# Optimization experiments

Hardware: AMD Instinct MI355X
Metric: run time of the kernel (lower is better)

The kernel has to match this reference:

```python
import jax, jax.numpy as jnp
import numpy as np

# Dropout layers are treated as identity (eval mode); note the original Adaptive
# module references self.dropout without defining it, so train mode would error anyway.

def setup_inputs() -> dict:
    key = jax.random.key(0)
    ks = jax.random.split(key, 13)
    B, T, H, E2, VOC, K = 128, 64, 512, 1024, 10000, 49
    s = lambda *sh: 1.0 / np.sqrt(sh[-1])
    return {
        "x":       jax.random.normal(ks[0], (B, T, E2), jnp.float32),
        "hiddens": jax.random.normal(ks[1], (B, T, H), jnp.float32),
        "cells":   jax.random.normal(ks[2], (B, T, H), jnp.float32),
        "V":       jax.random.normal(ks[3], (B, K, H), jnp.float32),
        # attention params
        "Wv": jax.random.normal(ks[4], (K, H), jnp.float32) * s(K, H),
        "Wg": jax.random.normal(ks[5], (K, H), jnp.float32) * s(K, H),
        "Ws": jax.random.normal(ks[6], (K, H), jnp.float32) * s(K, H),
        "wh": jax.random.normal(ks[7], (K,), jnp.float32) * s(K,),
        # sentinel params
        "Wx":  jax.random.normal(ks[8], (H, E2), jnp.float32) * s(H, E2),
        "Wsh": jax.random.normal(ks[9], (H, H), jnp.float32) * s(H, H),
        # output mlp
        "Wm": jax.random.normal(ks[10], (VOC, H), jnp.float32) * s(VOC, H),
        "bm": jnp.zeros((VOC,), jnp.float32),
    }


def reference(x, hiddens, cells, V, Wv, Wg, Ws, wh, Wx, Wsh, Wm, bm):
    B, T, H = hiddens.shape
    # h_{t-1}: zero init state prepended, last hidden dropped
    h0 = jnp.zeros((B, 1, H), hiddens.dtype)
    hiddens_t_1 = jnp.concatenate([h0, hiddens[:, :-1, :]], axis=1) if T > 1 else h0

    # Sentinel gate: sent_t = sigmoid(x Wx^T + h_{t-1} Wh^T) * tanh(cells)
    gate = jnp.einsum('bte,he->bth', x, Wx) + jnp.einsum('btj,hj->bth', hiddens_t_1, Wsh)
    sent = jax.nn.sigmoid(gate) * jnp.tanh(cells)            # [B,T,H]

    # Additive attention over K=49 spatial features
    cv = jnp.einsum('bkh,nh->bkn', V, Wv)                    # [B,K,49]
    cg = jnp.einsum('bth,nh->btn', hiddens, Wg)              # [B,T,49]
    content = jnp.tanh(cv[:, None, :, :] + cg[:, :, None, :])  # [B,T,K,49]
    z = jnp.einsum('btkn,n->btk', content, wh)               # [B,T,K]
    alpha = jax.nn.softmax(z, axis=-1)                       # [B,T,K]
    c = jnp.einsum('btk,bkh->bth', alpha, V)                 # [B,T,H]

    # Sentinel-extended softmax -> beta
    cs = jnp.einsum('bth,nh->btn', sent, Ws) + cg            # [B,T,49]
    z_ext = jnp.einsum('btn,n->bt', jnp.tanh(cs), wh)[..., None]  # [B,T,1]
    extend = jnp.concatenate([z, z_ext], axis=-1)            # [B,T,K+1]
    alpha_hat = jax.nn.softmax(extend, axis=-1)
    beta = alpha_hat[:, :, -1:]                              # [B,T,1]

    c_hat = beta * sent + (1.0 - beta) * c                   # [B,T,H]
    output = jnp.einsum('bth,vh->btv', c_hat + hiddens, Wm) + bm  # [B,T,vocab]
    return output, alpha, beta
```

## Files before the change

### kernel.cpp

```cpp
#include <hip/hip_runtime.h>
#include <hip/hip_bf16.h>
#include <math.h>

typedef __bf16 bf16;
typedef __bf16 bf16x4 __attribute__((ext_vector_type(4)));
typedef __bf16 bf16x8 __attribute__((ext_vector_type(8)));
typedef float f32x4 __attribute__((ext_vector_type(4)));

#define BB  128
#define TT  64
#define BTT 8192
#define HH  512
#define EE  1024
#define KA  49
#define NV  10000

__device__ __forceinline__ float ftanh(float x) {
    float cx = fminf(fmaxf(x, -15.f), 15.f);
    float e = __expf(2.f * cx);
    return (e - 1.f) * __builtin_amdgcn_rcpf(e + 1.f);
}
__device__ __forceinline__ float fsigmoid(float x) {
    return __builtin_amdgcn_rcpf(1.f + __expf(-x));
}

__device__ __forceinline__ void cvt4(const float* __restrict__ s, bf16* __restrict__ d) {
    f32x4 v = *(const f32x4*)s;
    bf16x4 o = { (bf16)v[0], (bf16)v[1], (bf16)v[2], (bf16)v[3] };
    *(bf16x4*)d = o;
}
__device__ __forceinline__ void cvt4nt(const float* __restrict__ s, bf16* __restrict__ d) {
    f32x4 v = __builtin_nontemporal_load((const f32x4*)s);
    bf16x4 o = { (bf16)v[0], (bf16)v[1], (bf16)v[2], (bf16)v[3] };
    *(bf16x4*)d = o;
}

__global__ __launch_bounds__(256)
void prep_kernel(const float* __restrict__ hid,
                 const float* __restrict__ V, const float* __restrict__ Wv,
                 const float* __restrict__ Wg, const float* __restrict__ Ws,
                 const float* __restrict__ Wx, const float* __restrict__ Wsh,
                 bf16* __restrict__ hb,
                 bf16* __restrict__ Vb, bf16* __restrict__ Wvb, bf16* __restrict__ Wgb,
                 bf16* __restrict__ Wsb, bf16* __restrict__ Wxb, bf16* __restrict__ Wshb,
                 bf16* __restrict__ zbuf)
{
    if (blockIdx.x == 0 && threadIdx.x < 128) {
        bf16x8 z = {};
        *(bf16x8*)(zbuf + threadIdx.x * 8) = z;
    }

    const long NH = (long)BTT * HH;
    const long NVV = (long)BB * KA * HH;
    const long NWX = (long)HH * EE;
    const long NWSH = (long)HH * HH;
    const long NW = (long)KA * HH;
    const long total4 = (NH + NVV + NWX + NWSH + 3 * NW) >> 2;

    long t0 = (long)blockIdx.x * 256 + threadIdx.x;
    long st = (long)gridDim.x * 256;
    for (long i4 = t0; i4 < total4; i4 += st) {
        long i = i4 << 2;
        if (i < NH) { cvt4(hid + i, hb + i); continue; }
        i -= NH;
        if (i < NVV) { cvt4nt(V + i, Vb + i); continue; }
        i -= NVV;
        if (i < NWX) { cvt4nt(Wx + i, Wxb + i); continue; }
        i -= NWX;
        if (i < NWSH) { cvt4nt(Wsh + i, Wshb + i); continue; }
        i -= NWSH;
        if (i < NW) { cvt4nt(Wv + i, Wvb + i); continue; }
        i -= NW;
        if (i < NW) { cvt4nt(Wg + i, Wgb + i); continue; }
        i -= NW;
        cvt4nt(Ws + i, Wsb + i);
    }
}

template<int EPI, bool SHIFT>
__device__ __forceinline__ void gemm128_core(
    bf16* smem,
    const bf16* __restrict__ A1, const bf16* __restrict__ B1, int K1,
    const bf16* __restrict__ A2, const bf16* __restrict__ B2, int K2,
    int N, const float* __restrict__ eaux, void* __restrict__ outv, int ldo,
    int bm0, int bn0, const bf16* __restrict__ zbuf)
{
    const int tid = threadIdx.x;
    const int lane = tid & 63;
    const int wid = tid >> 6;
    const int wm = (wid >> 1) * 64;
    const int wn = (wid & 1) * 64;
    const int rA = lane & 15;
    const int ks = lane >> 4;
    const int swzB = (ks ^ ((rA >> 1) & 3)) * 16;

    const int c0 = tid, c1 = tid + 256;
    const int row0 = c0 >> 2, row1 = c1 >> 2;
    const int gc0 = ((c0 & 3) ^ ((row0 >> 1) & 3)) * 8;
    const int gc1 = ((c1 & 3) ^ ((row1 >> 1) & 3)) * 8;
    const int br0 = (bn0 + row0 < N) ? bn0 + row0 : N - 1;
    const int br1 = (bn0 + row1 < N) ? bn0 + row1 : N - 1;

    const int NT1 = K1 >> 5;
    const int NT2 = K2 >> 5;
    const int NT = NT1 + NT2;

    const bf16* A1r0 = A1 + (size_t)(bm0 + row0) * K1 + gc0;
    const bf16* A1r1 = A1 + (size_t)(bm0 + row1) * K1 + gc1;
    const bf16* B1r0 = B1 + (size_t)br0 * K1 + gc0;
    const bf16* B1r1 = B1 + (size_t)br1 * K1 + gc1;
    const bf16 *A2r0 = nullptr, *A2r1 = nullptr, *B2r0 = nullptr, *B2r1 = nullptr;
    if (K2 > 0) {
        if (SHIFT) {
            A2r0 = (((bm0 + row0) & 63) == 0) ? zbuf + gc0
                                              : A2 + (size_t)(bm0 + row0 - 1) * K2 + gc0;
            A2r1 = (((bm0 + row1) & 63) == 0) ? zbuf + gc1
                                              : A2 + (size_t)(bm0 + row1 - 1) * K2 + gc1;
        } else {
            A2r0 = A2 + (size_t)(bm0 + row0) * K2 + gc0;
            A2r1 = A2 + (size_t)(bm0 + row1) * K2 + gc1;
        }
        B2r0 = B2 + (size_t)br0 * K2 + gc0;
        B2r1 = B2 + (size_t)br1 * K2 + gc1;
    }

    auto stage = [&](int t) {
        const bf16 *a0, *a1, *b0, *b1; int k0;
        if (t < NT1) { k0 = t << 5;          a0 = A1r0; a1 = A1r1; b0 = B1r0; b1 = B1r1; }
        else         { k0 = (t - NT1) << 5;  a0 = A2r0; a1 = A2r1; b0 = B2r0; b1 = B2r1; }
        char* base = (char*)smem + (t & 3) * 16384;
        __builtin_amdgcn_global_load_lds(
            (const __attribute__((address_space(1))) unsigned int*)(a0 + k0),
            (__attribute__((address_space(3))) unsigned int*)(base + c0 * 16), 16, 0, 0);
        __builtin_amdgcn_global_load_lds(
            (const __attribute__((address_space(1))) unsigned int*)(a1 + k0),
            (__attribute__((address_space(3))) unsigned int*)(base + c1 * 16), 16, 0, 0);
        __builtin_amdgcn_global_load_lds(
            (const __attribute__((address_space(1))) unsigned int*)(b0 + k0),
            (__attribute__((address_space(3))) unsigned int*)(base + 8192 + c0 * 16), 16, 0, 0);
        __builtin_amdgcn_global_load_lds(
            (const __attribute__((address_space(1))) unsigned int*)(b1 + k0),
            (__attribute__((address_space(3))) unsigned int*)(base + 8192 + c1 * 16), 16, 0, 0);
    };

    f32x4 acc[4][4] = {};

    stage(0); stage(1); stage(2);
    asm volatile("s_waitcnt vmcnt(8)" ::: "memory");
    __builtin_amdgcn_s_barrier();

    for (int t = 0; t < NT; ++t) {
        const char* sA = (const char*)smem + (t & 3) * 16384;
        const char* sB = sA + 8192;

        bf16x8 af[4], bfr[4];
        #pragma unroll
        for (int mi = 0; mi < 4; ++mi)
            af[mi] = *(const bf16x8*)(sA + (wm + mi * 16 + rA) * 64 + swzB);
        #pragma unroll
        for (int ni = 0; ni < 4; ++ni)
            bfr[ni] = *(const bf16x8*)(sB + (wn + ni * 16 + rA) * 64 + swzB);

        if (t + 3 < NT) {
            stage(t + 3);
            asm volatile("s_waitcnt vmcnt(8)" ::: "memory");
        } else if (t + 2 < NT) {
            asm volatile("s_waitcnt vmcnt(4)" ::: "memory");
        } else {
            asm volatile("s_waitcnt vmcnt(0)" ::: "memory");
        }
        __builtin_amdgcn_s_barrier();

        __builtin_amdgcn_s_setprio(1);
        #pragma unroll
        for (int mi = 0; mi < 4; ++mi) {
            #pragma unroll
            for (int ni = 0; ni < 4; ++ni)
                acc[mi][ni] = __builtin_amdgcn_mfma_f32_16x16x32_bf16(af[mi], bfr[ni], acc[mi][ni], 0, 0, 0);
        }
        __builtin_amdgcn_s_setprio(0);
        __builtin_amdgcn_s_barrier();
    }

    #pragma unroll
    for (int mi = 0; mi < 4; ++mi) {
        #pragma unroll
        for (int ni = 0; ni < 4; ++ni) {
            const int col = bn0 + wn + ni * 16 + rA;
            if (col < N) {
                #pragma unroll
                for (int r = 0; r < 4; ++r) {
                    const int rowg = bm0 + wm + mi * 16 + ks * 4 + r;
                    float v = acc[mi][ni][r];
                    if (EPI == 0) {
                        ((bf16*)outv)[(size_t)rowg * ldo + col] =
                            (bf16)(fsigmoid(v) * ftanh(eaux[(size_t)rowg * ldo + col]));
                    } else {
                        ((float*)outv)[(size_t)rowg * ldo + col] = v;
                    }
                }
            }
        }
    }
}

__device__ __forceinline__ void gate128f(
    char* smem, const float* __restrict__ xf, const bf16* __restrict__ Wxb,
    const bf16* __restrict__ hb, const bf16* __restrict__ Wshb,
    const float* __restrict__ cel, bf16* __restrict__ sentb,
    int bm0, int bn0, const bf16* __restrict__ zbuf)
{
    const int NT1 = EE >> 5;
    const int NT = NT1 + (HH >> 5);

    const int tid = threadIdx.x;
    const int lane = tid & 63;
    const int wid = tid >> 6;
    const int wm = (wid >> 1) * 64;
    const int wn = (wid & 1) * 64;
    const int rA = lane & 15;
    const int ks = lane >> 4;
    const int swzB = (ks ^ ((rA >> 1) & 3)) * 16;

    const float* xsrc[4];
    #pragma unroll
    for (int j = 0; j < 4; ++j) {
        const int c = tid + 256 * j;
        const int row = c >> 3, slot = c & 7;
        xsrc[j] = xf + (size_t)(bm0 + row) * EE + ((slot ^ ((row >> 1) & 7)) << 2);
    }
    const int cb0 = tid, cb1 = tid + 256;
    const int brow0 = cb0 >> 2, brow1 = cb1 >> 2;
    const int gb0 = ((cb0 & 3) ^ ((brow0 >> 1) & 3)) * 8;
    const int gb1 = ((cb1 & 3) ^ ((brow1 >> 1) & 3)) * 8;

    const bf16* B1r0 = Wxb + (size_t)(bn0 + brow0) * EE + gb0;
    const bf16* B1r1 = Wxb + (size_t)(bn0 + brow1) * EE + gb1;
    const bf16* B2r0 = Wshb + (size_t)(bn0 + brow0) * HH + gb0;
    const bf16* B2r1 = Wshb + (size_t)(bn0 + brow1) * HH + gb1;
    const bf16* A2r0 = (((bm0 + brow0) & 63) == 0) ? zbuf + gb0
                                                   : hb + (size_t)(bm0 + brow0 - 1) * HH + gb0;
    const bf16* A2r1 = (((bm0 + brow1) & 63) == 0) ? zbuf + gb1
                                                   : hb + (size_t)(bm0 + brow1 - 1) * HH + gb1;

    auto stage = [&](int t, int slot) {
        char* base = smem + slot * 24576;
        if (t < NT1) {
            const int k0 = t << 5;
            #pragma unroll
            for (int j = 0; j < 4; ++j)
                __builtin_amdgcn_global_load_lds(
                    (const __attribute__((address_space(1))) unsigned int*)(xsrc[j] + k0),
                    (__attribute__((address_space(3))) unsigned int*)(base + (tid + 256 * j) * 16), 16, 0, 0);
            __builtin_amdgcn_global_load_lds(
                (const __attribute__((address_space(1))) unsigned int*)(B1r0 + k0),
                (__attribute__((address_space(3))) unsigned int*)(base + 16384 + cb0 * 16), 16, 0, 0);
            __builtin_amdgcn_global_load_lds(
                (const __attribute__((address_space(1))) unsigned int*)(B1r1 + k0),
                (__attribute__((address_space(3))) unsigned int*)(base + 16384 + cb1 * 16), 16, 0, 0);
        } else {
            const int k0 = (t - NT1) << 5;
            __builtin_amdgcn_global_load_lds(
                (const __attribute__((address_space(1))) unsigned int*)(A2r0 + k0),
                (__attribute__((address_space(3))) unsigned int*)(base + cb0 * 16), 16, 0, 0);
            __builtin_amdgcn_global_load_lds(
                (const __attribute__((address_space(1))) unsigned int*)(A2r1 + k0),
                (__attribute__((address_space(3))) unsigned int*)(base + cb1 * 16), 16, 0, 0);
            __builtin_amdgcn_global_load_lds(
                (const __attribute__((address_space(1))) unsigned int*)(B2r0 + k0),
                (__attribute__((address_space(3))) unsigned int*)(base + 16384 + cb0 * 16), 16, 0, 0);
            __builtin_amdgcn_global_load_lds(
                (const __attribute__((address_space(1))) unsigned int*)(B2r1 + k0),
                (__attribute__((address_space(3))) unsigned int*)(base + 16384 + cb1 * 16), 16, 0, 0);
        }
    };

    f32x4 acc[4][4] = {};

    stage(0, 0); stage(1, 1);
    asm volatile("s_waitcnt vmcnt(6)" ::: "memory");
    __builtin_amdgcn_s_barrier();

    int slR = 0, slS = 2;
    for (int t = 0; t < NT; ++t) {
        const char* base = smem + slR * 24576;
        const char* sB = base + 16384;

        bf16x8 af[4], bfr[4];
        if (t < NT1) {
            #pragma unroll
            for (int mi = 0; mi < 4; ++mi) {
                const int row = wm + mi * 16 + rA;
                const int m = (row >> 1) & 7;
                f32x4 lo = *(const f32x4*)(base + row * 128 + (((2 * ks) ^ m) << 4));
                f32x4 hi = *(const f32x4*)(base + row * 128 + (((2 * ks + 1) ^ m) << 4));
                bf16x8 v = { (bf16)lo[0], (bf16)lo[1], (bf16)lo[2], (bf16)lo[3],
                             (bf16)hi[0], (bf16)hi[1], (bf16)hi[2], (bf16)hi[3] };
                af[mi] = v;
            }
        } else {
            #pragma unroll
            for (int mi = 0; mi < 4; ++mi)
                af[mi] = *(const bf16x8*)(base + (wm + mi * 16 + rA) * 64 + swzB);
        }
        #pragma unroll
        for (int ni = 0; ni < 4; ++ni)
            bfr[ni] = *(const bf16x8*)(sB + (wn + ni * 16 + rA) * 64 + swzB);

        if (t + 2 < NT) {
            stage(t + 2, slS);
            if (t + 2 < NT1) asm volatile("s_waitcnt vmcnt(6)" ::: "memory");
            else             asm volatile("s_waitcnt vmcnt(4)" ::: "memory");
        } else {
            asm volatile("s_waitcnt vmcnt(0)" ::: "memory");
        }
        __builtin_amdgcn_s_barrier();

        __builtin_amdgcn_s_setprio(1);
        #pragma unroll
        for (int mi = 0; mi < 4; ++mi) {
            #pragma unroll
            for (int ni = 0; ni < 4; ++ni)
                acc[mi][ni] = __builtin_amdgcn_mfma_f32_16x16x32_bf16(af[mi], bfr[ni], acc[mi][ni], 0, 0, 0);
        }
        __builtin_amdgcn_s_setprio(0);
        __builtin_amdgcn_s_barrier();

        slR = (slR == 2) ? 0 : slR + 1;
        slS = (slS == 2) ? 0 : slS + 1;
    }

    #pragma unroll
    for (int mi = 0; mi < 4; ++mi) {
        #pragma unroll
        for (int ni = 0; ni < 4; ++ni) {
            const int col = bn0 + wn + ni * 16 + rA;
            #pragma unroll
            for (int r = 0; r < 4; ++r) {
                const int rowg = bm0 + wm + mi * 16 + ks * 4 + r;
                sentb[(size_t)rowg * HH + col] =
                    (bf16)(fsigmoid(acc[mi][ni][r]) * ftanh(cel[(size_t)rowg * HH + col]));
            }
        }
    }
}

__global__ __launch_bounds__(256, 2)
void gate_mid128(const float* __restrict__ xf, const bf16* __restrict__ Wxb,
                 const bf16* __restrict__ Wshb,
                 const float* __restrict__ cel, bf16* __restrict__ sentb,
                 const bf16* __restrict__ Vb, const bf16* __restrict__ Wvb,
                 const bf16* __restrict__ hb, const bf16* __restrict__ Wgb,
                 float* __restrict__ cv, float* __restrict__ cg,
                 const float* __restrict__ Wm, bf16* __restrict__ Wmb,
                 const bf16* __restrict__ zbuf)
{
    __shared__ char smem[73728];
    const int bid = blockIdx.x;
    if (bid >= 369) {
        const long n4 = ((long)NV * HH) >> 2;
        for (long i4 = (long)(bid - 369) * 256 + threadIdx.x; i4 < n4; i4 += 143L * 256)
            cvt4nt(Wm + (i4 << 2), Wmb + (i4 << 2));
        return;
    }
    if (bid < 256) {
        const int lin = (bid & 7) * 32 + (bid >> 3);
        gate128f(smem, xf, Wxb, hb, Wshb, cel, sentb,
                 (lin >> 2) * 128, (lin & 3) * 128, zbuf);
    } else if (bid < 305) {
        gemm128_core<2, false>((bf16*)smem, Vb, Wvb, HH, nullptr, nullptr, 0, KA, nullptr,
                               (void*)cv, KA, (bid - 256) * 128, 0, nullptr);
    } else {
        gemm128_core<2, false>((bf16*)smem, hb, Wgb, HH, nullptr, nullptr, 0, KA, nullptr,
                               (void*)cg, KA, (bid - 305) * 128, 0, nullptr);
    }
}

__global__ __launch_bounds__(256, 2)
void cs64(const bf16* __restrict__ sentb, const bf16* __restrict__ Wsb,
          float* __restrict__ cs)
{
    __shared__ bf16 smem[4 * 4096];
    const int bm0 = blockIdx.x * 64;
    const int tid = threadIdx.x;
    const int lane = tid & 63;
    const int w = tid >> 6;
    const int rA = lane & 15;
    const int ks = lane >> 4;
    const int swzB = (ks ^ ((rA >> 1) & 3)) * 16;

    const int row = tid >> 2;
    const int gc = ((tid & 3) ^ ((row >> 1) & 3)) * 8;
    const int browc = (row < KA) ? row : KA - 1;
    const bf16* Ar = sentb + (size_t)(bm0 + row) * HH + gc;
    const bf16* Br = Wsb + (size_t)browc * HH + gc;

    auto stage = [&](int t) {
        char* base = (char*)smem + (t & 3) * 8192;
        const int k0 = t << 5;
        __builtin_amdgcn_global_load_lds(
            (const __attribute__((address_space(1))) unsigned int*)(Ar + k0),
            (__attribute__((address_space(3))) unsigned int*)(base + tid * 16), 16, 0, 0);
        __builtin_amdgcn_global_load_lds(
            (const __attribute__((address_space(1))) unsigned int*)(Br + k0),
            (__attribute__((address_space(3))) unsigned int*)(base + 4096 + tid * 16), 16, 0, 0);
    };

    f32x4 acc[4] = {};
    const int NT = HH / 32;

    stage(0); stage(1); stage(2);
    asm volatile("s_waitcnt vmcnt(4)" ::: "memory");
    __builtin_amdgcn_s_barrier();

    for (int t = 0; t < NT; ++t) {
        const char* sA = (const char*)smem + (t & 3) * 8192;
        const char* sB = sA + 4096;

        bf16x8 af[4];
        #pragma unroll
        for (int mi = 0; mi < 4; ++mi)
            af[mi] = *(const bf16x8*)(sA + (mi * 16 + rA) * 64 + swzB);
        bf16x8 bfr = *(const bf16x8*)(sB + (w * 16 + rA) * 64 + swzB);

        if (t + 3 < NT) {
            stage(t + 3);
            asm volatile("s_waitcnt vmcnt(4)" ::: "memory");
        } else if (t + 2 < NT) {
            asm volatile("s_waitcnt vmcnt(2)" ::: "memory");
        } else {
            asm volatile("s_waitcnt vmcnt(0)" ::: "memory");
        }
        __builtin_amdgcn_s_barrier();

        __builtin_amdgcn_s_setprio(1);
        #pragma unroll
        for (int mi = 0; mi < 4; ++mi)
            acc[mi] = __builtin_amdgcn_mfma_f32_16x16x32_bf16(af[mi], bfr, acc[mi], 0, 0, 0);
        __builtin_amdgcn_s_setprio(0);
        __builtin_amdgcn_s_barrier();
    }

    const int col = w * 16 + rA;
    if (col < KA) {
        #pragma unroll
        for (int mi = 0; mi < 4; ++mi) {
            #pragma unroll
            for (int r = 0; r < 4; ++r) {
                const int rowg = bm0 + mi * 16 + ks * 4 + r;
                cs[(size_t)rowg * KA + col] = acc[mi][r];
            }
        }
    }
}

__global__ __launch_bounds__(256)
void softz_kernel(const float* __restrict__ cv, const float* __restrict__ cg,
                  const float* __restrict__ cs, const float* __restrict__ wh,
                  float* __restrict__ alpha, float* __restrict__ beta)
{
    __shared__ float cvL[KA * KA];
    __shared__ float whL[64];
    __shared__ float cgL[4 * KA];

    const int tid = threadIdx.x;
    const int w = tid >> 6, lane = tid & 63;
    const int bt0 = blockIdx.x * 4;
    const int b = bt0 >> 6;
    const int bt = bt0 + w;

    const float* cvb = cv + (size_t)b * KA * KA;
    for (int i = tid; i < KA * KA; i += 256) cvL[i] = cvb[i];
    if (tid < KA) whL[tid] = wh[tid];
    if (lane < KA) cgL[w * KA + lane] = cg[(size_t)bt * KA + lane];
    float csv0 = (lane < KA) ? cs[(size_t)bt * KA + lane] : 0.f;
    __syncthreads();

    float z = -INFINITY;
    if (lane < KA) {
        const float* cvk = cvL + lane * KA;
        const float* cgr = cgL + w * KA;
        float acc = 0.f;
        #pragma unroll 7
        for (int n = 0; n < KA; ++n)
            acc += ftanh(cvk[n] + cgr[n]) * whL[n];
        z = acc;
    }
    const float csv = csv0 + ((lane < KA) ? cgL[w * KA + lane] : 0.f);
    float u = (lane < KA) ? ftanh(csv) * whL[lane] : 0.f;

    float m1 = z;
    #pragma unroll
    for (int o = 32; o; o >>= 1) m1 = fmaxf(m1, __shfl_xor(m1, o, 64));
    float e = (lane < KA) ? __expf(z - m1) : 0.f;
    float s1 = e, ze = u;
    #pragma unroll
    for (int o = 32; o; o >>= 1) { s1 += __shfl_xor(s1, o, 64); ze += __shfl_xor(ze, o, 64); }

    if (lane < KA) alpha[(size_t)bt * KA + lane] = e / s1;
    if (lane == 0) {
        float M2 = fmaxf(m1, ze);
        float denom = s1 * __expf(m1 - M2) + __expf(ze - M2);
        beta[bt] = __expf(ze - M2) / denom;
    }
}

__global__ __launch_bounds__(256)
void cch_kernel(const float* __restrict__ alpha, const float* __restrict__ beta,
                const bf16* __restrict__ Vb, const bf16* __restrict__ sentb,
                const float* __restrict__ hid, bf16* __restrict__ chb)
{
    __shared__ float aL[TT * KA];
    __shared__ float bL[TT];

    const int b = blockIdx.x >> 3;
    const int hc = blockIdx.x & 7;
    const int tid = threadIdx.x;
    const int w = tid >> 6, lane = tid & 63;
    const int h = hc * 64 + lane;

    const float* ab = alpha + (size_t)b * TT * KA;
    for (int i = tid; i < TT * KA; i += 256) aL[i] = ab[i];
    if (tid < TT) bL[tid] = beta[b * TT + tid];

    float vreg[KA];
    #pragma unroll
    for (int k = 0; k < KA; ++k) vreg[k] = (float)Vb[((size_t)b * KA + k) * HH + h];
    __syncthreads();

    #pragma unroll 1
    for (int tt = 0; tt < 16; ++tt) {
        const int t = w * 16 + tt;
        const int bt = b * TT + t;
        const float* ar = aL + t * KA;
        float c = 0.f;
        #pragma unroll
        for (int k = 0; k < KA; ++k) c += ar[k] * vreg[k];
        const float be = bL[t];
        const size_t idx = (size_t)bt * HH + h;
        float ch = be * (float)sentb[idx] + (1.f - be) * c
                 + __builtin_nontemporal_load(hid + idx);
        chb[idx] = (bf16)ch;
    }
}

__global__ __launch_bounds__(512, 4)
void gemm256x128_bias(const bf16* __restrict__ A, const bf16* __restrict__ B,
                      const float* __restrict__ bias, float* __restrict__ out)
{
    const int K = HH;
    const int N = NV;
    const int NT = K / 32;
    const int ntn = 79;

    __shared__ bf16 smem[3 * 12288];

    const int bid = blockIdx.x;
    const int wg = (bid & 7) * 316 + (bid >> 3);
    const int bm0 = (wg / ntn) * 256;
    const int bn0 = (wg % ntn) * 128;

    const int tid = threadIdx.x;
    const int lane = tid & 63;
    const int wid = tid >> 6;
    const int wr = (wid >> 1) * 64;
    const int wc = (wid & 1) * 64;
    const int rA = lane & 15;
    const int ks = lane >> 4;
    const int swz = (ks ^ ((rA >> 1) & 3)) * 16;

    const int arow0 = tid >> 2;
    const int arow1 = arow0 + 128;
    const int gcA0 = ((tid & 3) ^ ((arow0 >> 1) & 3)) * 8;
    const int gcA1 = ((tid & 3) ^ ((arow1 >> 1) & 3)) * 8;
    const int brow = tid >> 2;
    const int gcB  = ((tid & 3) ^ ((brow >> 1) & 3)) * 8;
    const int browc = (bn0 + brow < N) ? bn0 + brow : N - 1;

    const bf16* Ap0 = A + (size_t)(bm0 + arow0) * K + gcA0;
    const bf16* Ap1 = A + (size_t)(bm0 + arow1) * K + gcA1;
    const bf16* Bp  = B + (size_t)browc * K + gcB;

    auto stage = [&](int t, int slot) {
        char* base = (char*)smem + slot * 24576;
        const int k0 = t << 5;
        __builtin_amdgcn_global_load_lds(
            (const __attribute__((address_space(1))) unsigned int*)(Ap0 + k0),
            (__attribute__((address_space(3))) unsigned int*)(base + tid * 16), 16, 0, 0);
        __builtin_amdgcn_global_load_lds(
            (const __attribute__((address_space(1))) unsigned int*)(Ap1 + k0),
            (__attribute__((address_space(3))) unsigned int*)(base + (tid + 512) * 16), 16, 0, 0);
        __builtin_amdgcn_global_load_lds(
            (const __attribute__((address_space(1))) unsigned int*)(Bp + k0),
            (__attribute__((address_space(3))) unsigned int*)(base + 16384 + tid * 16), 16, 0, 0);
    };

    f32x4 acc[4][4] = {};

    stage(0, 0); stage(1, 1);
    asm volatile("s_waitcnt vmcnt(3)" ::: "memory");
    __builtin_amdgcn_s_barrier();

    int slR = 0, slS = 2;
    for (int t = 0; t < NT; ++t) {
        const char* sA = (const char*)smem + slR * 24576;
        const char* sB = sA + 16384;

        bf16x8 af[4], bfr[4];
        #pragma unroll
        for (int mi = 0; mi < 4; ++mi)
            af[mi] = *(const bf16x8*)(sA + (wr + mi * 16 + rA) * 64 + swz);
        #pragma unroll
        for (int ni = 0; ni < 4; ++ni)
            bfr[ni] = *(const bf16x8*)(sB + (wc + ni * 16 + rA) * 64 + swz);

        if (t + 2 < NT) {
            stage(t + 2, slS);
            asm volatile("s_waitcnt vmcnt(3)" ::: "memory");
        } else {
            asm volatile("s_waitcnt vmcnt(0)" ::: "memory");
        }
        __builtin_amdgcn_s_barrier();

        __builtin_amdgcn_s_setprio(1);
        #pragma unroll
        for (int mi = 0; mi < 4; ++mi) {
            #pragma unroll
            for (int ni = 0; ni < 4; ++ni)
                acc[mi][ni] = __builtin_amdgcn_mfma_f32_16x16x32_bf16(af[mi], bfr[ni], acc[mi][ni], 0, 0, 0);
        }
        __builtin_amdgcn_s_setprio(0);
        __builtin_amdgcn_s_barrier();

        slR = (slR == 2) ? 0 : slR + 1;
        slS = (slS == 2) ? 0 : slS + 1;
    }

    float bv[4];
    #pragma unroll
    for (int ni = 0; ni < 4; ++ni) {
        const int col = bn0 + wc + ni * 16 + rA;
        bv[ni] = (col < N) ? bias[col] : 0.f;
    }
    float* lt = (float*)smem + wid * 2048;
    #pragma unroll
    for (int half = 0; half < 2; ++half) {
        #pragma unroll
        for (int mi2 = 0; mi2 < 2; ++mi2) {
            const int mi = half * 2 + mi2;
            #pragma unroll
            for (int ni = 0; ni < 4; ++ni) {
                #pragma unroll
                for (int r = 0; r < 4; ++r) {
                    const int row = mi2 * 16 + ks * 4 + r;
                    const int col = ni * 16 + rA;
                    const int s = ((((row >> 2) & 3) ^ (row & 3)) << 4);
                    lt[row * 64 + (col ^ s)] = acc[mi][ni][r] + bv[ni];
                }
            }
        }
        #pragma unroll
        for (int i = 0; i < 8; ++i) {
            const int row = i * 4 + ks;
            const int c0 = rA * 4;
            const int s = ((((row >> 2) & 3) ^ (row & 3)) << 4);
            f32x4 v = *(const f32x4*)&lt[row * 64 + (c0 ^ s)];
            const int rowg = bm0 + wr + half * 32 + row;
            const int colg = bn0 + wc + c0;
            if (colg < N)
                __builtin_nontemporal_store(v, (f32x4*)&out[(size_t)rowg * N + colg]);
        }
    }
}

extern "C" void kernel_launch(void* const* d_in, const int* in_sizes, int n_in,
                              void* d_out, int out_size, void* d_ws, size_t ws_size,
                              hipStream_t stream)
{
    const float* x   = (const float*)d_in[0];
    const float* hid = (const float*)d_in[1];
    const float* cel = (const float*)d_in[2];
    const float* V   = (const float*)d_in[3];
    const float* Wv  = (const float*)d_in[4];
    const float* Wg  = (const float*)d_in[5];
    const float* Ws  = (const float*)d_in[6];
    const float* wh  = (const float*)d_in[7];
    const float* Wx  = (const float*)d_in[8];
    const float* Wsh = (const float*)d_in[9];
    const float* Wm  = (const float*)d_in[10];
    const float* bm  = (const float*)d_in[11];

    float* out_o   = (float*)d_out;
    float* alpha_o = out_o + (size_t)BTT * NV;
    float* beta_o  = alpha_o + (size_t)BTT * KA;

    char* p = (char*)d_ws;
    bf16* sentb = (bf16*)p; p += (size_t)BTT * HH * 2;
    bf16* chb   = (bf16*)p; p += (size_t)BTT * HH * 2;
    bf16* hb    = (bf16*)p; p += (size_t)BTT * HH * 2;
    bf16* Vb    = (bf16*)p; p += (size_t)BB * KA * HH * 2;
    bf16* Wxb   = (bf16*)p; p += (size_t)HH * EE * 2;
    bf16* Wshb  = (bf16*)p; p += (size_t)HH * HH * 2;
    bf16* Wmb   = (bf16*)p; p += (size_t)NV * HH * 2;
    bf16* Wvb   = (bf16*)p; p += (size_t)KA * HH * 2;
    bf16* Wgb   = (bf16*)p; p += (size_t)KA * HH * 2;
    bf16* Wsb   = (bf16*)p; p += (size_t)KA * HH * 2;
    bf16* zbuf  = (bf16*)p; p += 1024 * 2;
    float* cv   = (float*)p; p += (size_t)BB * KA * KA * 4;
    float* cg   = (float*)p; p += (size_t)BTT * KA * 4;
    float* cs   = (float*)p; p += (size_t)BTT * KA * 4;

    prep_kernel<<<2048, 256, 0, stream>>>(hid, V, Wv, Wg, Ws, Wx, Wsh,
                                          hb, Vb, Wvb, Wgb, Wsb, Wxb, Wshb, zbuf);

    gate_mid128<<<512, 256, 0, stream>>>(x, Wxb, Wshb, cel, sentb,
                                         Vb, Wvb, hb, Wgb, cv, cg, Wm, Wmb, zbuf);

    cs64<<<128, 256, 0, stream>>>(sentb, Wsb, cs);

    softz_kernel<<<BTT / 4, 256, 0, stream>>>(cv, cg, cs, wh, alpha_o, beta_o);
    cch_kernel<<<BB * 8, 256, 0, stream>>>(alpha_o, beta_o, Vb, sentb, hid, chb);

    gemm256x128_bias<<<32 * 79, 512, 0, stream>>>(chb, Wmb, bm, out_o);
}
```

Baseline: 206.0 us.

## Compute attention logits concurrently with cs GEMM in a merged launch

Moves the expensive tanh-based attention logit computation (z) out of the softmax kernel and into extra blocks of the cs GEMM launch, so the 128 GEMM blocks and 2048 logit blocks share one grid. The logits go to a new workspace buffer, and a slimmer softmax kernel reads z, cg and cs to produce alpha and beta. The aim is to fill the GPU while the small cs GEMM runs and shorten the serial chain. It adds an extra global round-trip for z and one more buffer.

```diff
diff --git a/kernel.cpp b/kernel.cpp
--- a/kernel.cpp
+++ b/kernel.cpp
@@ -377,12 +377,44 @@
 }
 
 __global__ __launch_bounds__(256, 2)
-void cs64(const bf16* __restrict__ sentb, const bf16* __restrict__ Wsb,
-          float* __restrict__ cs)
-{
-    __shared__ bf16 smem[4 * 4096];
-    const int bm0 = blockIdx.x * 64;
+void cs_z(const bf16* __restrict__ sentb, const bf16* __restrict__ Wsb,
+          float* __restrict__ cs,
+          const float* __restrict__ cv, const float* __restrict__ cg,
+          const float* __restrict__ wh, float* __restrict__ zb)
+{
+    __shared__ char sm[32768];
+    const int bid = blockIdx.x;
     const int tid = threadIdx.x;
+
+    if (bid >= 128) {
+        float* cvL = (float*)sm;
+        float* whL = (float*)(sm + 9604);
+        float* cgL = (float*)(sm + 9860);
+        const int w = tid >> 6, lane = tid & 63;
+        const int bt0 = (bid - 128) * 4;
+        const int b = bt0 >> 6;
+        const int bt = bt0 + w;
+
+        const float* cvb = cv + (size_t)b * KA * KA;
+        for (int i = tid; i < KA * KA; i += 256) cvL[i] = cvb[i];
+        if (tid < KA) whL[tid] = wh[tid];
+        if (lane < KA) cgL[w * KA + lane] = cg[(size_t)bt * KA + lane];
+        __syncthreads();
+
+        if (lane < KA) {
+            const float* cvk = cvL + lane * KA;
+            const float* cgr = cgL + w * KA;
+            float acc = 0.f;
+            #pragma unroll 7
+            for (int n = 0; n < KA; ++n)
+                acc += ftanh(cvk[n] + cgr[n]) * whL[n];
+            zb[(size_t)bt * KA + lane] = acc;
+        }
+        return;
+    }
+
+    bf16* smem = (bf16*)sm;
+    const int bm0 = bid * 64;
     const int lane = tid & 63;
     const int w = tid >> 6;
     const int rA = lane & 15;
@@ -455,39 +487,23 @@
 }
 
 __global__ __launch_bounds__(256)
-void softz_kernel(const float* __restrict__ cv, const float* __restrict__ cg,
-                  const float* __restrict__ cs, const float* __restrict__ wh,
-                  float* __restrict__ alpha, float* __restrict__ beta)
-{
-    __shared__ float cvL[KA * KA];
+void softz2_kernel(const float* __restrict__ zb, const float* __restrict__ cg,
+                   const float* __restrict__ cs, const float* __restrict__ wh,
+                   float* __restrict__ alpha, float* __restrict__ beta)
+{
     __shared__ float whL[64];
-    __shared__ float cgL[4 * KA];
 
     const int tid = threadIdx.x;
     const int w = tid >> 6, lane = tid & 63;
-    const int bt0 = blockIdx.x * 4;
-    const int b = bt0 >> 6;
-    const int bt = bt0 + w;
-
-    const float* cvb = cv + (size_t)b * KA * KA;
-    for (int i = tid; i < KA * KA; i += 256) cvL[i] = cvb[i];
+    const int bt = blockIdx.x * 4 + w;
+
     if (tid < KA) whL[tid] = wh[tid];
-    if (lane < KA) cgL[w * KA + lane] = cg[(size_t)bt * KA + lane];
-    float csv0 = (lane < KA) ? cs[(size_t)bt * KA + lane] : 0.f;
+    const float cgv = (lane < KA) ? cg[(size_t)bt * KA + lane] : 0.f;
+    const float csv0 = (lane < KA) ? cs[(size_t)bt * KA + lane] : 0.f;
+    const float z = (lane < KA) ? zb[(size_t)bt * KA + lane] : -INFINITY;
     __syncthreads();
 
-    float z = -INFINITY;
-    if (lane < KA) {
-        const float* cvk = cvL + lane * KA;
-        const float* cgr = cgL + w * KA;
-        float acc = 0.f;
-        #pragma unroll 7
-        for (int n = 0; n < KA; ++n)
-            acc += ftanh(cvk[n] + cgr[n]) * whL[n];
-        z = acc;
-    }
-    const float csv = csv0 + ((lane < KA) ? cgL[w * KA + lane] : 0.f);
-    float u = (lane < KA) ? ftanh(csv) * whL[lane] : 0.f;
+    float u = (lane < KA) ? ftanh(csv0 + cgv) * whL[lane] : 0.f;
 
     float m1 = z;
     #pragma unroll
@@ -709,6 +725,7 @@
     float* cv   = (float*)p; p += (size_t)BB * KA * KA * 4;
     float* cg   = (float*)p; p += (size_t)BTT * KA * 4;
     float* cs   = (float*)p; p += (size_t)BTT * KA * 4;
+    float* zb   = (float*)p; p += (size_t)BTT * KA * 4;
 
     prep_kernel<<<2048, 256, 0, stream>>>(hid, V, Wv, Wg, Ws, Wx, Wsh,
                                           hb, Vb, Wvb, Wgb, Wsb, Wxb, Wshb, zbuf);
@@ -716,9 +733,9 @@
     gate_mid128<<<512, 256, 0, stream>>>(x, Wxb, Wshb, cel, sentb,
                                          Vb, Wvb, hb, Wgb, cv, cg, Wm, Wmb, zbuf);
 
-    cs64<<<128, 256, 0, stream>>>(sentb, Wsb, cs);
-
-    softz_kernel<<<BTT / 4, 256, 0, stream>>>(cv, cg, cs, wh, alpha_o, beta_o);
+    cs_z<<<128 + BTT / 4, 256, 0, stream>>>(sentb, Wsb, cs, cv, cg, wh, zb);
+
+    softz2_kernel<<<BTT / 4, 256, 0, stream>>>(zb, cg, cs, wh, alpha_o, beta_o);
     cch_kernel<<<BB * 8, 256, 0, stream>>>(alpha_o, beta_o, Vb, sentb, hid, chb);
 
     gemm256x128_bias<<<32 * 79, 512, 0, stream>>>(chb, Wmb, bm, out_o);
```

Result: no change. 207.9 us (+0.9%).
